# Optimization experiments

Hardware: AMD Instinct MI355X
Metric: run time of the kernel (lower is better)

## Reference

```python
import jax, jax.numpy as jnp
import numpy as np

N_HEAD = 16

def setup_inputs() -> dict:
    key = jax.random.key(0)
    ks = jax.random.split(key, 9)
    B, T, C = 8, 1023, 1024
    d_k = C // N_HEAD
    return {
        "x": jax.random.normal(ks[0], (B, T, C), dtype=jnp.float32),
        "w1_w": jax.random.normal(ks[1], (C, C), dtype=jnp.float32) * 0.02,
        "w1_b": jax.random.normal(ks[2], (C,), dtype=jnp.float32) * 0.02,
        "w2": jax.random.uniform(ks[3], (d_k, T), dtype=jnp.float32, minval=-0.001, maxval=0.001),
        "b2": jax.random.normal(ks[4], (T,), dtype=jnp.float32) * 0.02,
        "value_w": jax.random.normal(ks[5], (C, C), dtype=jnp.float32) * 0.02,
        "value_b": jax.random.normal(ks[6], (C,), dtype=jnp.float32) * 0.02,
        "proj_w": jax.random.normal(ks[7], (C, C), dtype=jnp.float32) * 0.02,
        "proj_b": jax.random.normal(ks[8], (C,), dtype=jnp.float32) * 0.02,
    }

def reference(x, w1_w, w1_b, w2, b2, value_w, value_b, proj_w, proj_b):
    B, T, C = x.shape
    H = N_HEAD
    d_k = C // H
    relu_out = jax.nn.relu(x @ w1_w.T + w1_b).reshape(B, T, H, d_k).transpose(0, 2, 1, 3)
    v = (x @ value_w.T + value_b).reshape(B, T, H, d_k).transpose(0, 2, 1, 3)
    # synthesized scores: [B,H,T,M] with M = block_size-1, then slice to T
    scores = jnp.einsum('bhtd,dm->bhtm', relu_out, w2) + b2
    scores = scores[:, :, :T, :T]
    causal = jnp.tril(jnp.ones((T, T), dtype=bool))
    scores = jnp.where(causal, scores, jnp.float32(-1e10))
    prob = jax.nn.softmax(scores, axis=-1)
    y = jnp.einsum('bhts,bhsd->bhtd', prob, v)
    y = y.transpose(0, 2, 1, 3).reshape(B, T, C)
    return y @ proj_w.T + proj_b
```

## Files before the change

### kernel.cpp

```cpp
#include <hip/hip_runtime.h>
#include <hip/hip_bf16.h>

#define N_HEAD 16

typedef __hip_bfloat16 bf16;
typedef __attribute__((ext_vector_type(4))) float f32x4;
typedef __attribute__((ext_vector_type(8))) short bf16x8;

__device__ __forceinline__ float bf2f(unsigned short u) {
    union { unsigned int i; float f; } v; v.i = ((unsigned int)u) << 16; return v.f;
}
__device__ __forceinline__ unsigned short f2bf(float f) {
    union { float f; unsigned int i; } v; v.f = f;
    unsigned int x = v.i;
    unsigned int r = x + 0x7fffu + ((x >> 16) & 1u);
    return (unsigned short)(r >> 16);
}
__device__ __forceinline__ void gload_lds16(const bf16* g, bf16* l) {
    __builtin_amdgcn_global_load_lds(
        (const __attribute__((address_space(1))) void*)g,
        (__attribute__((address_space(3))) void*)l, 16, 0, 0);
}

__global__ __launch_bounds__(256)
void k_split(const float* __restrict__ src, bf16* __restrict__ dst,
             int Mreal, int loseg)
{
    const int idx = blockIdx.x * 256 + threadIdx.x;
    const int r   = idx / 768;
    const int c   = (idx - r * 768) * 4;
    const int seg = c >> 10;
    const int sc  = c & 1023;
    float4 v = (r < Mreal) ? *(const float4*)(src + (size_t)r * 1024 + sc)
                           : make_float4(0.f, 0.f, 0.f, 0.f);
    const float* pv = &v.x;
    unsigned short o[4];
#pragma unroll
    for (int j = 0; j < 4; ++j) {
        unsigned short h = f2bf(pv[j]);
        o[j] = (seg == loseg) ? f2bf(pv[j] - bf2f(h)) : h;
    }
    *(ushort4*)((unsigned short*)dst + (size_t)r * 3072 + c) =
        make_ushort4(o[0], o[1], o[2], o[3]);
}

__global__ __launch_bounds__(256)
void k_w2t(const float* __restrict__ w2, bf16* __restrict__ w2t)
{
    const int idx = blockIdx.x * 256 + threadIdx.x;
    const int t = idx >> 6;
    const int d = idx & 63;
    float v = (t < 1023) ? w2[d * 1023 + t] : 0.f;
    ((unsigned short*)w2t)[idx] = f2bf(v);
}

__global__ __launch_bounds__(256)
void gemm_split(const bf16* __restrict__ X, const bf16* __restrict__ W,
                const float* __restrict__ bias, float* __restrict__ outF,
                bf16* __restrict__ outB, bf16* __restrict__ outVT,
                int Kd, int N, int Mstore, int relu)
{
    constexpr int BK = 32;
    __shared__ bf16 sA[2][128 * BK];
    __shared__ bf16 sB[2][128 * BK];

    const int tid = threadIdx.x;
    const int l   = tid & 63;
    const int wv  = tid >> 6;
    const int wr  = (wv >> 1) * 64;
    const int wc  = (wv & 1) * 64;
    const int lr  = l & 15;
    const int lk  = (l >> 4) * 8;

    const int m0 = blockIdx.x * 128;
    const int n0 = blockIdx.y * 128;

    const int r0 = tid >> 2;
    const int c0 = (tid & 3) * 8;
    const bf16* gA0 = X + (size_t)(m0 + r0) * Kd + c0;
    const bf16* gA1 = X + (size_t)(m0 + 64 + r0) * Kd + c0;
    const bf16* gB0 = W + (size_t)(n0 + r0) * Kd + c0;
    const bf16* gB1 = W + (size_t)(n0 + 64 + r0) * Kd + c0;
    const int wb0 = wv * 512;
    const int wb1 = 2048 + wv * 512;

    f32x4 acc[4][4];
#pragma unroll
    for (int i = 0; i < 4; ++i)
#pragma unroll
        for (int j = 0; j < 4; ++j) {
            f32x4 z = {0.f, 0.f, 0.f, 0.f};
            acc[i][j] = z;
        }

    gload_lds16(gA0, &sA[0][wb0]);
    gload_lds16(gA1, &sA[0][wb1]);
    gload_lds16(gB0, &sB[0][wb0]);
    gload_lds16(gB1, &sB[0][wb1]);
    __syncthreads();

    const int nt = Kd / BK;
    int cur = 0;
    for (int t = 0; t < nt; ++t) {
        if (t + 1 < nt) {
            const int ko = (t + 1) * BK;
            gload_lds16(gA0 + ko, &sA[cur ^ 1][wb0]);
            gload_lds16(gA1 + ko, &sA[cur ^ 1][wb1]);
            gload_lds16(gB0 + ko, &sB[cur ^ 1][wb0]);
            gload_lds16(gB1 + ko, &sB[cur ^ 1][wb1]);
        }
        bf16x8 af[4], bfr[4];
#pragma unroll
        for (int i = 0; i < 4; ++i)
            af[i] = *(const bf16x8*)&sA[cur][(wr + i * 16 + lr) * BK + lk];
#pragma unroll
        for (int j = 0; j < 4; ++j)
            bfr[j] = *(const bf16x8*)&sB[cur][(wc + j * 16 + lr) * BK + lk];
#pragma unroll
        for (int i = 0; i < 4; ++i)
#pragma unroll
            for (int j = 0; j < 4; ++j)
                acc[i][j] = __builtin_amdgcn_mfma_f32_16x16x32_bf16(
                    af[i], bfr[j], acc[i][j], 0, 0, 0);
        __syncthreads();
        cur ^= 1;
    }

    float bv[4];
#pragma unroll
    for (int j = 0; j < 4; ++j) bv[j] = bias[n0 + wc + j * 16 + lr];

    if (outB) {
        unsigned short* ob = (unsigned short*)outB;
#pragma unroll
        for (int i = 0; i < 4; ++i)
#pragma unroll
            for (int r = 0; r < 4; ++r) {
                const int row = m0 + wr + i * 16 + (l >> 4) * 4 + r;
#pragma unroll
                for (int j = 0; j < 4; ++j) {
                    float v = acc[i][j][r] + bv[j];
                    if (relu) v = fmaxf(v, 0.f);
                    ob[(size_t)row * N + n0 + wc + j * 16 + lr] = f2bf(v);
                }
            }
    } else if (outVT) {
        unsigned short* ov = (unsigned short*)outVT;
#pragma unroll
        for (int i = 0; i < 4; ++i)
#pragma unroll
            for (int r = 0; r < 4; ++r) {
                const int row = m0 + wr + i * 16 + (l >> 4) * 4 + r;
                if (row < 8184) {
                    const int bb = row / 1023;
                    const int t  = row - bb * 1023;
#pragma unroll
                    for (int j = 0; j < 4; ++j) {
                        const int n = n0 + wc + j * 16 + lr;
                        float v = acc[i][j][r] + bv[j];
                        ov[((size_t)(bb * 16 + (n >> 6)) * 64 + (n & 63)) * 1024 + t]
                            = f2bf(v);
                    }
                }
            }
    } else {
#pragma unroll
        for (int i = 0; i < 4; ++i)
#pragma unroll
            for (int r = 0; r < 4; ++r) {
                const int row = m0 + wr + i * 16 + (l >> 4) * 4 + r;
                if (row < Mstore)
#pragma unroll
                    for (int j = 0; j < 4; ++j)
                        outF[(size_t)row * N + n0 + wc + j * 16 + lr] =
                            acc[i][j][r] + bv[j];
            }
    }
}

__global__ __launch_bounds__(256)
void synth_attn_mfma(const bf16* __restrict__ A, const bf16* __restrict__ VT,
                     const bf16* __restrict__ W2T, const float* __restrict__ b2,
                     bf16* __restrict__ Ys)
{
    constexpr int T = 1023, C = 1024;
    const int tt = blockIdx.x, h = blockIdx.y, b = blockIdx.z;
    const int tid = threadIdx.x;
    const int w  = tid >> 6;
    const int l  = tid & 63;
    const int lr = l & 15;
    const int lg = l >> 4;
    const int qbase = tt * 64 + w * 16;

    __shared__ unsigned short sP[4][16 * 64];
    char* myP = (char*)&sP[w][0];

    bf16x8 af0, af1;
    {
        const bf16* ap = A + (size_t)(b * T + qbase + lr) * C + h * 64 + lg * 8;
        af0 = *(const bf16x8*)(ap);
        af1 = *(const bf16x8*)(ap + 32);
    }

    f32x4 accY[4];
#pragma unroll
    for (int fd = 0; fd < 4; ++fd) { f32x4 z = {0,0,0,0}; accY[fd] = z; }
    float mrun[4], lrun[4];
#pragma unroll
    for (int r = 0; r < 4; ++r) { mrun[r] = -INFINITY; lrun[r] = 0.f; }

    const bf16* vbase = VT + (size_t)(b * 16 + h) * 64 * 1024;

    for (int kt = 0; kt <= tt; ++kt) {
        const int m0 = kt * 64;

        bf16x8 wf[4][2];
#pragma unroll
        for (int fm = 0; fm < 4; ++fm) {
            const bf16* p = W2T + (size_t)(m0 + fm * 16 + lr) * 64 + lg * 8;
            wf[fm][0] = *(const bf16x8*)(p);
            wf[fm][1] = *(const bf16x8*)(p + 32);
        }
        float b2v[4];
#pragma unroll
        for (int fm = 0; fm < 4; ++fm) {
            const int m = m0 + fm * 16 + lr;
            b2v[fm] = (m < T) ? b2[m] : 0.f;
        }

        f32x4 s[4];
#pragma unroll
        for (int fm = 0; fm < 4; ++fm) {
            f32x4 z = {0,0,0,0};
            z = __builtin_amdgcn_mfma_f32_16x16x32_bf16(af0, wf[fm][0], z, 0, 0, 0);
            z = __builtin_amdgcn_mfma_f32_16x16x32_bf16(af1, wf[fm][1], z, 0, 0, 0);
            s[fm] = z;
        }

        bf16x8 vf[4][2];
#pragma unroll
        for (int fd = 0; fd < 4; ++fd) {
            const bf16* p = vbase + (size_t)(fd * 16 + lr) * 1024 + m0 + lg * 8;
            vf[fd][0] = *(const bf16x8*)(p);
            vf[fd][1] = *(const bf16x8*)(p + 32);
        }

        float sv[4][4];
#pragma unroll
        for (int fm = 0; fm < 4; ++fm) {
            const int m = m0 + fm * 16 + lr;
#pragma unroll
            for (int r = 0; r < 4; ++r) {
                const int t = qbase + lg * 4 + r;
                float x = s[fm][r] + b2v[fm];
                sv[fm][r] = (m > t) ? -1e30f : x;
            }
        }
#pragma unroll
        for (int r = 0; r < 4; ++r) {
            float rm = fmaxf(fmaxf(sv[0][r], sv[1][r]), fmaxf(sv[2][r], sv[3][r]));
#pragma unroll
            for (int off = 8; off >= 1; off >>= 1)
                rm = fmaxf(rm, __shfl_xor(rm, off, 16));
            const float mnew = fmaxf(mrun[r], rm);
            const float sc = __expf(mrun[r] - mnew);
            float ps = 0.f;
#pragma unroll
            for (int fm = 0; fm < 4; ++fm) {
                float p = __expf(sv[fm][r] - mnew);
                sv[fm][r] = p;
                ps += p;
            }
#pragma unroll
            for (int off = 8; off >= 1; off >>= 1)
                ps += __shfl_xor(ps, off, 16);
            lrun[r] = lrun[r] * sc + ps;
            mrun[r] = mnew;
#pragma unroll
            for (int fd = 0; fd < 4; ++fd) accY[fd][r] *= sc;
        }

#pragma unroll
        for (int r = 0; r < 4; ++r) {
            const int row = lg * 4 + r;
            const int swz = (row & 7) << 4;
#pragma unroll
            for (int fm = 0; fm < 4; ++fm) {
                const int byte = (row * 128 + (fm * 16 + lr) * 2) ^ swz;
                *(unsigned short*)(myP + byte) = f2bf(sv[fm][r]);
            }
        }
        bf16x8 pa0, pa1;
        {
            const int swz = (lr & 7) << 4;
            pa0 = *(const bf16x8*)(myP + ((lr * 128 + lg * 16) ^ swz));
            pa1 = *(const bf16x8*)(myP + ((lr * 128 + 64 + lg * 16) ^ swz));
        }

#pragma unroll
        for (int fd = 0; fd < 4; ++fd) {
            accY[fd] = __builtin_amdgcn_mfma_f32_16x16x32_bf16(pa0, vf[fd][0], accY[fd], 0, 0, 0);
            accY[fd] = __builtin_amdgcn_mfma_f32_16x16x32_bf16(pa1, vf[fd][1], accY[fd], 0, 0, 0);
        }
    }

#pragma unroll
    for (int r = 0; r < 4; ++r) {
        const int t = qbase + lg * 4 + r;
        if (t >= T) continue;
        const float inv = 1.f / lrun[r];
        unsigned short* dst = (unsigned short*)Ys + (size_t)(b * T + t) * 3072 + h * 64 + lr;
#pragma unroll
        for (int fd = 0; fd < 4; ++fd) {
            const float y = accY[fd][r] * inv;
            const unsigned short hi = f2bf(y);
            const unsigned short lo = f2bf(y - bf2f(hi));
            dst[fd * 16]        = hi;
            dst[fd * 16 + 1024] = lo;
            dst[fd * 16 + 2048] = hi;
        }
    }
}

extern "C" void kernel_launch(void* const* d_in, const int* in_sizes, int n_in,
                              void* d_out, int out_size, void* d_ws, size_t ws_size,
                              hipStream_t stream)
{
    const float* x       = (const float*)d_in[0];
    const float* w1_w    = (const float*)d_in[1];
    const float* w1_b    = (const float*)d_in[2];
    const float* w2      = (const float*)d_in[3];
    const float* b2      = (const float*)d_in[4];
    const float* value_w = (const float*)d_in[5];
    const float* value_b = (const float*)d_in[6];
    const float* proj_w  = (const float*)d_in[7];
    const float* proj_b  = (const float*)d_in[8];
    float* out = (float*)d_out;

    const int B = 8, T = 1023, C = 1024;
    const int BT = B * T;
    const int Mp = 8192;
    const int Ks = 3072;

    bf16* xs   = (bf16*)d_ws;
    bf16* w1s  = xs   + (size_t)Mp * Ks;
    bf16* vws  = w1s  + (size_t)1024 * Ks;
    bf16* pws  = vws  + (size_t)1024 * Ks;
    bf16* Abuf = pws  + (size_t)1024 * Ks;
    bf16* VTb  = Abuf + (size_t)Mp * 1024;
    bf16* w2T  = VTb  + (size_t)B * 16 * 64 * 1024;

    k_split<<<(Mp * 768) / 256, 256, 0, stream>>>(x, xs, BT, 1);
    k_split<<<(1024 * 768) / 256, 256, 0, stream>>>(w1_w, w1s, 1024, 2);
    k_split<<<(1024 * 768) / 256, 256, 0, stream>>>(value_w, vws, 1024, 2);
    k_split<<<(1024 * 768) / 256, 256, 0, stream>>>(proj_w, pws, 1024, 2);
    k_w2t<<<256, 256, 0, stream>>>(w2, w2T);

    dim3 gg(Mp / 128, C / 128);
    gemm_split<<<gg, 256, 0, stream>>>(xs, w1s, w1_b, nullptr, Abuf, nullptr, Ks, C, Mp, 1);
    gemm_split<<<gg, 256, 0, stream>>>(xs, vws, value_b, nullptr, nullptr, VTb, Ks, C, Mp, 0);

    dim3 ag(16, N_HEAD, B);
    synth_attn_mfma<<<ag, 256, 0, stream>>>(Abuf, VTb, w2T, b2, xs);

    gemm_split<<<gg, 256, 0, stream>>>(xs, pws, proj_b, out, nullptr, nullptr, Ks, C, BT, 0);
}
```

Baseline: 579.8 us.

## Drop online-softmax max tracking, prefetch W2 tiles, reverse tile order in attention

```diff
diff --git a/kernel.cpp b/kernel.cpp
--- a/kernel.cpp
+++ b/kernel.cpp
@@ -184,7 +184,8 @@
                      bf16* __restrict__ Ys)
 {
     constexpr int T = 1023, C = 1024;
-    const int tt = blockIdx.x, h = blockIdx.y, b = blockIdx.z;
+    const int tt = (int)gridDim.x - 1 - (int)blockIdx.x;
+    const int h = blockIdx.y, b = blockIdx.z;
     const int tid = threadIdx.x;
     const int w  = tid >> 6;
     const int l  = tid & 63;
@@ -204,111 +205,111 @@
 
     f32x4 accY[4];
 #pragma unroll
-    for (int fd = 0; fd < 4; ++fd) { f32x4 z = {0,0,0,0}; accY[fd] = z; }
-    float mrun[4], lrun[4];
-#pragma unroll
-    for (int r = 0; r < 4; ++r) { mrun[r] = -INFINITY; lrun[r] = 0.f; }
+    for (int fd = 0; fd < 4; ++fd) { f32x4 z = {0.f,0.f,0.f,0.f}; accY[fd] = z; }
+    f32x4 psum = {0.f, 0.f, 0.f, 0.f};
 
     const bf16* vbase = VT + (size_t)(b * 16 + h) * 64 * 1024;
 
-    for (int kt = 0; kt <= tt; ++kt) {
-        const int m0 = kt * 64;
-
-        bf16x8 wf[4][2];
-#pragma unroll
-        for (int fm = 0; fm < 4; ++fm) {
-            const bf16* p = W2T + (size_t)(m0 + fm * 16 + lr) * 64 + lg * 8;
-            wf[fm][0] = *(const bf16x8*)(p);
-            wf[fm][1] = *(const bf16x8*)(p + 32);
-        }
-        float b2v[4];
-#pragma unroll
-        for (int fm = 0; fm < 4; ++fm) {
-            const int m = m0 + fm * 16 + lr;
-            b2v[fm] = (m < T) ? b2[m] : 0.f;
-        }
-
-        f32x4 s[4];
-#pragma unroll
-        for (int fm = 0; fm < 4; ++fm) {
-            f32x4 z = {0,0,0,0};
-            z = __builtin_amdgcn_mfma_f32_16x16x32_bf16(af0, wf[fm][0], z, 0, 0, 0);
-            z = __builtin_amdgcn_mfma_f32_16x16x32_bf16(af1, wf[fm][1], z, 0, 0, 0);
-            s[fm] = z;
-        }
-
-        bf16x8 vf[4][2];
-#pragma unroll
-        for (int fd = 0; fd < 4; ++fd) {
-            const bf16* p = vbase + (size_t)(fd * 16 + lr) * 1024 + m0 + lg * 8;
-            vf[fd][0] = *(const bf16x8*)(p);
-            vf[fd][1] = *(const bf16x8*)(p + 32);
-        }
-
-        float sv[4][4];
-#pragma unroll
-        for (int fm = 0; fm < 4; ++fm) {
-            const int m = m0 + fm * 16 + lr;
-#pragma unroll
-            for (int r = 0; r < 4; ++r) {
-                const int t = qbase + lg * 4 + r;
-                float x = s[fm][r] + b2v[fm];
-                sv[fm][r] = (m > t) ? -1e30f : x;
-            }
-        }
-#pragma unroll
-        for (int r = 0; r < 4; ++r) {
-            float rm = fmaxf(fmaxf(sv[0][r], sv[1][r]), fmaxf(sv[2][r], sv[3][r]));
-#pragma unroll
-            for (int off = 8; off >= 1; off >>= 1)
-                rm = fmaxf(rm, __shfl_xor(rm, off, 16));
-            const float mnew = fmaxf(mrun[r], rm);
-            const float sc = __expf(mrun[r] - mnew);
-            float ps = 0.f;
-#pragma unroll
-            for (int fm = 0; fm < 4; ++fm) {
-                float p = __expf(sv[fm][r] - mnew);
-                sv[fm][r] = p;
-                ps += p;
-            }
-#pragma unroll
-            for (int off = 8; off >= 1; off >>= 1)
-                ps += __shfl_xor(ps, off, 16);
-            lrun[r] = lrun[r] * sc + ps;
-            mrun[r] = mnew;
-#pragma unroll
-            for (int fd = 0; fd < 4; ++fd) accY[fd][r] *= sc;
-        }
-
-#pragma unroll
-        for (int r = 0; r < 4; ++r) {
-            const int row = lg * 4 + r;
-            const int swz = (row & 7) << 4;
-#pragma unroll
-            for (int fm = 0; fm < 4; ++fm) {
-                const int byte = (row * 128 + (fm * 16 + lr) * 2) ^ swz;
-                *(unsigned short*)(myP + byte) = f2bf(sv[fm][r]);
-            }
-        }
-        bf16x8 pa0, pa1;
+    bf16x8 wfA[4][2], wfB[4][2];
+    float b2A[4], b2B[4];
+
+#define LOADW(KT, WF, B2V) do {                                               \
+    const int _w0 = (KT) * 64;                                                \
+    _Pragma("unroll")                                                         \
+    for (int fm = 0; fm < 4; ++fm) {                                          \
+        const bf16* _p = W2T + (size_t)(_w0 + fm * 16 + lr) * 64 + lg * 8;    \
+        WF[fm][0] = *(const bf16x8*)(_p);                                     \
+        WF[fm][1] = *(const bf16x8*)(_p + 32);                                \
+        const int _m = _w0 + fm * 16 + lr;                                    \
+        B2V[fm] = (_m < T) ? b2[_m] : 0.f;                                    \
+    } } while (0)
+
+#define STEP_PRE(KT, WF)                                                      \
+    const int _km0 = (KT) * 64;                                               \
+    bf16x8 vf[4][2];                                                          \
+    _Pragma("unroll")                                                         \
+    for (int fd = 0; fd < 4; ++fd) {                                          \
+        const bf16* _p = vbase + (size_t)(fd * 16 + lr) * 1024 + _km0 + lg * 8; \
+        vf[fd][0] = *(const bf16x8*)(_p);                                     \
+        vf[fd][1] = *(const bf16x8*)(_p + 32);                                \
+    }                                                                         \
+    f32x4 s[4];                                                               \
+    __builtin_amdgcn_s_setprio(1);                                            \
+    _Pragma("unroll")                                                         \
+    for (int fm = 0; fm < 4; ++fm) {                                          \
+        f32x4 _z = {0.f, 0.f, 0.f, 0.f};                                      \
+        _z = __builtin_amdgcn_mfma_f32_16x16x32_bf16(af0, WF[fm][0], _z, 0, 0, 0); \
+        _z = __builtin_amdgcn_mfma_f32_16x16x32_bf16(af1, WF[fm][1], _z, 0, 0, 0); \
+        s[fm] = _z;                                                           \
+    }                                                                         \
+    __builtin_amdgcn_s_setprio(0);
+
+#define STEP_POST(B2V) do {                                                   \
+    float _pv[4][4];                                                          \
+    _Pragma("unroll")                                                         \
+    for (int fm = 0; fm < 4; ++fm) {                                          \
+        const int _m = _km0 + fm * 16 + lr;                                   \
+        _Pragma("unroll")                                                     \
+        for (int r = 0; r < 4; ++r) {                                         \
+            const int _t = qbase + lg * 4 + r;                                \
+            const float _e = __expf(s[fm][r] + B2V[fm]);                      \
+            const float _p = (_m > _t) ? 0.f : _e;                            \
+            _pv[fm][r] = _p;                                                  \
+            psum[r] += _p;                                                    \
+        }                                                                     \
+    }                                                                         \
+    _Pragma("unroll")                                                         \
+    for (int r = 0; r < 4; ++r) {                                             \
+        const int _row = lg * 4 + r;                                          \
+        const int _swz = (_row & 7) << 4;                                     \
+        _Pragma("unroll")                                                     \
+        for (int fm = 0; fm < 4; ++fm) {                                      \
+            const int _byte = (_row * 128 + (fm * 16 + lr) * 2) ^ _swz;       \
+            *(unsigned short*)(myP + _byte) = f2bf(_pv[fm][r]);               \
+        }                                                                     \
+    }                                                                         \
+    bf16x8 _pa0, _pa1;                                                        \
+    {                                                                         \
+        const int _sw = (lr & 7) << 4;                                        \
+        _pa0 = *(const bf16x8*)(myP + ((lr * 128 + lg * 16) ^ _sw));          \
+        _pa1 = *(const bf16x8*)(myP + ((lr * 128 + 64 + lg * 16) ^ _sw));     \
+    }                                                                         \
+    __builtin_amdgcn_s_setprio(1);                                            \
+    _Pragma("unroll")                                                         \
+    for (int fd = 0; fd < 4; ++fd) {                                          \
+        accY[fd] = __builtin_amdgcn_mfma_f32_16x16x32_bf16(_pa0, vf[fd][0], accY[fd], 0, 0, 0); \
+        accY[fd] = __builtin_amdgcn_mfma_f32_16x16x32_bf16(_pa1, vf[fd][1], accY[fd], 0, 0, 0); \
+    }                                                                         \
+    __builtin_amdgcn_s_setprio(0);                                            \
+    } while (0)
+
+    LOADW(0, wfA, b2A);
+    for (int kt = 0; kt <= tt; kt += 2) {
         {
-            const int swz = (lr & 7) << 4;
-            pa0 = *(const bf16x8*)(myP + ((lr * 128 + lg * 16) ^ swz));
-            pa1 = *(const bf16x8*)(myP + ((lr * 128 + 64 + lg * 16) ^ swz));
-        }
-
-#pragma unroll
-        for (int fd = 0; fd < 4; ++fd) {
-            accY[fd] = __builtin_amdgcn_mfma_f32_16x16x32_bf16(pa0, vf[fd][0], accY[fd], 0, 0, 0);
-            accY[fd] = __builtin_amdgcn_mfma_f32_16x16x32_bf16(pa1, vf[fd][1], accY[fd], 0, 0, 0);
-        }
-    }
+            STEP_PRE(kt, wfA)
+            if (kt < tt) LOADW(kt + 1, wfB, b2B);
+            STEP_POST(b2A);
+        }
+        if (kt + 1 > tt) break;
+        {
+            STEP_PRE(kt + 1, wfB)
+            if (kt + 1 < tt) LOADW(kt + 2, wfA, b2A);
+            STEP_POST(b2B);
+        }
+    }
+#undef LOADW
+#undef STEP_PRE
+#undef STEP_POST
 
 #pragma unroll
     for (int r = 0; r < 4; ++r) {
+        float ps = psum[r];
+#pragma unroll
+        for (int off = 8; off >= 1; off >>= 1)
+            ps += __shfl_xor(ps, off, 16);
         const int t = qbase + lg * 4 + r;
         if (t >= T) continue;
-        const float inv = 1.f / lrun[r];
+        const float inv = 1.f / ps;
         unsigned short* dst = (unsigned short*)Ys + (size_t)(b * T + t) * 3072 + h * 64 + lr;
 #pragma unroll
         for (int fd = 0; fd < 4; ++fd) {
```

New measurement: 577.9 us. Within noise of the previous version (-0.3%).
